# Optimization experiments

Hardware: AMD Instinct MI355X
Metric: run time of the kernel (lower is better)

## Reference

```python
import jax, jax.numpy as jnp
import numpy as np

H = 32  # hidden_size

def _lstm_layer(x, Wih, Whh, bih, bhh):
    """Single LSTM layer, batch_first x: [B,T,I] -> hs [B,T,H].
    PyTorch gate order: i, f, g, o."""
    B = x.shape[0]
    # Precompute all input projections at once: [B,T,4H] -> time-major [T,B,4H]
    xp = (jnp.einsum('bti,gi->btg', x, Wih) + bih + bhh).transpose(1, 0, 2)
    h0 = jnp.zeros((B, H), dtype=x.dtype)
    c0 = jnp.zeros((B, H), dtype=x.dtype)

    def step(carry, xt):
        h, c = carry
        gates = xt + h @ Whh.T                      # [B,4H]
        i, f, g, o = jnp.split(gates, 4, axis=-1)
        i = jax.nn.sigmoid(i)
        f = jax.nn.sigmoid(f)
        g = jnp.tanh(g)
        o = jax.nn.sigmoid(o)
        c = f * c + i * g
        h = o * jnp.tanh(c)
        return (h, c), h

    _, hs = jax.lax.scan(step, (h0, c0), xp)        # hs: [T,B,H]
    return hs.transpose(1, 0, 2)                    # [B,T,H]


def setup_inputs() -> dict:
    key = jax.random.key(0)
    ks = jax.random.split(key, 12)
    B, T, I = 4096, 512, 1
    s = 1.0 / np.sqrt(H)  # PyTorch uniform(-1/sqrt(H), 1/sqrt(H)) init scale
    u = lambda k, shape: jax.random.uniform(k, shape, jnp.float32, -s, s)
    return {
        'x': jax.random.normal(ks[0], (B, T, I), jnp.float32),
        'W_ih_l0': u(ks[1], (4 * H, I)),
        'W_hh_l0': u(ks[2], (4 * H, H)),
        'b_ih_l0': u(ks[3], (4 * H,)),
        'b_hh_l0': u(ks[4], (4 * H,)),
        'W_ih_l1': u(ks[5], (4 * H, H)),
        'W_hh_l1': u(ks[6], (4 * H, H)),
        'b_ih_l1': u(ks[7], (4 * H,)),
        'b_hh_l1': u(ks[8], (4 * H,)),
        'W_fc': u(ks[9], (1, H)),
        'b_fc': u(ks[10], (1,)),
    }


def reference(x, W_ih_l0, W_hh_l0, b_ih_l0, b_hh_l0,
              W_ih_l1, W_hh_l1, b_ih_l1, b_hh_l1, W_fc, b_fc):
    h1 = _lstm_layer(x, W_ih_l0, W_hh_l0, b_ih_l0, b_hh_l0)   # [B,T,H]
    h2 = _lstm_layer(h1, W_ih_l1, W_hh_l1, b_ih_l1, b_hh_l1)  # [B,T,H]
    out = h2[:, -1, :] @ W_fc.T + b_fc                        # [B,1]
    return jax.nn.relu(out)
```

## Files before the change

kernel.cpp:

```cpp
#include <hip/hip_runtime.h>
#include <hip/hip_bf16.h>


typedef __attribute__((ext_vector_type(8))) short bf16x8;
typedef __attribute__((ext_vector_type(4))) float f32x4;
typedef __attribute__((ext_vector_type(4))) int   i32x4;

#define HID 32
#define SEQ 512
#define L2E 1.4426950408889634f
#define LSTR 20

static __device__ __forceinline__ float fexp2(float x){ return __builtin_amdgcn_exp2f(x); }
static __device__ __forceinline__ float frcp (float x){ return __builtin_amdgcn_rcpf(x); }
static __device__ __forceinline__ short f2bf(float f){
  unsigned u = __builtin_bit_cast(unsigned, f);
  u = (u + 0x7fffu + ((u >> 16) & 1u)) >> 16;
  return (short)u;
}

#define CELL(gi, gf, gg, go, cvr, hout) do {                         \
  const float I_ = fexp2(gi), G_ = fexp2(gg);                        \
  const float F_ = fexp2(gf), O_ = fexp2(go);                        \
  const float a_ = 1.f + I_, b_ = 1.f + G_, c_ = 1.f + F_;           \
  const float P1_ = a_ * b_;                                         \
  const float R_  = frcp(c_ * P1_);                                  \
  const float fv_ = P1_ * R_;                                        \
  const float ig_ = (G_ - 1.f) * (c_ * R_);                          \
  (cvr) = fmaf(fv_, (cvr), ig_);                                     \
  const float C2_ = fexp2((cvr) * (2.f * L2E));                      \
  (hout) = (C2_ - 1.f) * frcp((1.f + O_) * (1.f + C2_));             \
} while (0)

__global__ __launch_bounds__(512, 2) void lstm2_zs3_kernel(
    const float* __restrict__ x,
    const float* __restrict__ Wih0, const float* __restrict__ Whh0,
    const float* __restrict__ bih0, const float* __restrict__ bhh0,
    const float* __restrict__ Wih1, const float* __restrict__ Whh1,
    const float* __restrict__ bih1, const float* __restrict__ bhh1,
    const float* __restrict__ Wfc, const float* __restrict__ bfc,
    float* __restrict__ out)
{
  const int tid = threadIdx.x;
  const int w   = tid >> 6;
  const int l   = tid & 63;
  const int m   = l >> 4;
  const int col = l & 15;
  const int V   = w & 3;
  const bool isL1 = (w >= 4);

  __shared__ int   bufH0[4][16 * LSTR];
  __shared__ int   bufH1[2][16 * LSTR];
  __shared__ float bufFC[4][16];

  for (int i = tid; i < 4 * 16 * LSTR; i += 512) ((int*)bufH0)[i] = 0;
  for (int i = tid; i < 2 * 16 * LSTR; i += 512) ((int*)bufH1)[i] = 0;
  __syncthreads();

  const float* Wrec = isL1 ? Whh1 : Whh0;
  const float* Bi   = isL1 ? bih1 : bih0;
  const float* Bh   = isL1 ? bhh1 : bhh0;
  const int   gcol  = col & 3;
  const float scA   = (gcol == 2) ? (2.0f * L2E) : (-L2E);
  bf16x8 wfR[2], wfI[2];
  f32x4  cb[2];
  float  w0x[2][4];
  #pragma unroll
  for (int t = 0; t < 2; ++t) {
    const int ga = gcol * 32 + 8 * V + 2 * (col >> 2) + t;
    #pragma unroll
    for (int j = 0; j < 8; ++j) {
      wfR[t][j] = f2bf(scA * Wrec[ga * HID + (8 * m + j)]);
      wfI[t][j] = isL1 ? f2bf(scA * Wih1[ga * HID + (8 * m + j)]) : (short)0;
    }
    const int uc = 8 * V + 2 * m + t;
    #pragma unroll
    for (int rr = 0; rr < 4; ++rr) {
      const float sc = (rr == 2) ? (2.0f * L2E) : (-L2E);
      cb[t][rr]  = sc * (Bi[rr * 32 + uc] + Bh[rr * 32 + uc]);
      w0x[t][rr] = isL1 ? 0.f : sc * Wih0[rr * 32 + uc];
    }
  }
  const float wfcA = isL1 ? Wfc[8 * V + 2 * m]     : 0.f;
  const float wfcB = isL1 ? Wfc[8 * V + 2 * m + 1] : 0.f;

  float cvA = 0.f, cvB = 0.f, hA = 0.f, hB = 0.f;
  i32x4 h0pre = {0, 0, 0, 0};
  const float* xb = x + (size_t)(blockIdx.x * 16 + col) * SEQ;
  const int  rd = col * LSTR + 4 * m;
  const int  wb = col * LSTR + 4 * V + m;

  float4 xcur = {0.f, 0.f, 0.f, 0.f};
  if (!isL1) xcur = *reinterpret_cast<const float4*>(xb);

  for (int k = 0; k < SEQ / 4; ++k) {
    float4 xnext = {0.f, 0.f, 0.f, 0.f};
    if (!isL1 && k + 1 < SEQ / 4)
      xnext = *reinterpret_cast<const float4*>(xb + (k + 1) * 4);
    #pragma unroll
    for (int uu = 0; uu < 4; ++uu) {
      if (!isL1) {
        const i32x4 hv = *(const i32x4*)&bufH0[(uu + 3) & 3][rd];
        const bf16x8 hf = __builtin_bit_cast(bf16x8, hv);
        const float xt = (uu == 0) ? xcur.x : (uu == 1) ? xcur.y
                       : (uu == 2) ? xcur.z : xcur.w;
        f32x4 cbx0, cbx1;
        #pragma unroll
        for (int rr = 0; rr < 4; ++rr) {
          cbx0[rr] = fmaf(w0x[0][rr], xt, cb[0][rr]);
          cbx1[rr] = fmaf(w0x[1][rr], xt, cb[1][rr]);
        }
        f32x4 A0, A1;
        A0 = __builtin_amdgcn_mfma_f32_16x16x32_bf16(wfR[0], hf, cbx0, 0, 0, 0);
        A1 = __builtin_amdgcn_mfma_f32_16x16x32_bf16(wfR[1], hf, cbx1, 0, 0, 0);
        CELL(A0[0], A0[1], A0[2], A0[3], cvA, hA);
        CELL(A1[0], A1[1], A1[2], A1[3], cvB, hB);
        int pk;
        asm("v_cvt_pk_bf16_f32 %0, %1, %2" : "=v"(pk) : "v"(hA), "v"(hB));
        bufH0[uu][wb] = pk;
      } else {
        const bool doC = (uu >= 2) || (k > 0);
        const bool doP = (uu >= 1) || (k > 0);
        i32x4 h1v = {0, 0, 0, 0};
        if (doC) h1v = *(const i32x4*)&bufH1[(uu + 1) & 1][rd];
        i32x4 h0next = h0pre;
        if (doP) h0next = *(const i32x4*)&bufH0[(uu + 3) & 3][rd];
        if (doC) {
          const bf16x8 h0f = __builtin_bit_cast(bf16x8, h0pre);
          const bf16x8 h1f = __builtin_bit_cast(bf16x8, h1v);
          const f32x4 z4 = {0.f, 0.f, 0.f, 0.f};
          f32x4 P0, P1, Q0, Q1;
          __builtin_amdgcn_s_setprio(1);
          P0 = __builtin_amdgcn_mfma_f32_16x16x32_bf16(wfI[0], h0f, cb[0], 0, 0, 0);
          P1 = __builtin_amdgcn_mfma_f32_16x16x32_bf16(wfI[1], h0f, cb[1], 0, 0, 0);
          Q0 = __builtin_amdgcn_mfma_f32_16x16x32_bf16(wfR[0], h1f, z4, 0, 0, 0);
          Q1 = __builtin_amdgcn_mfma_f32_16x16x32_bf16(wfR[1], h1f, z4, 0, 0, 0);
          __builtin_amdgcn_s_setprio(0);
          const f32x4 A0 = P0 + Q0;
          const f32x4 A1 = P1 + Q1;
          CELL(A0[0], A0[1], A0[2], A0[3], cvA, hA);
          CELL(A1[0], A1[1], A1[2], A1[3], cvB, hB);
          int pk;
          asm("v_cvt_pk_bf16_f32 %0, %1, %2" : "=v"(pk) : "v"(hA), "v"(hB));
          bufH1[uu & 1][wb] = pk;
        }
        h0pre = h0next;
      }
      __syncthreads();
    }
    xcur = xnext;
  }

  if (isL1) {
    const i32x4 h1v = *(const i32x4*)&bufH1[1][rd];
    const bf16x8 h0f = __builtin_bit_cast(bf16x8, h0pre);
    const bf16x8 h1f = __builtin_bit_cast(bf16x8, h1v);
    f32x4 A0, A1;
    A0 = __builtin_amdgcn_mfma_f32_16x16x32_bf16(wfI[0], h0f, cb[0], 0, 0, 0);
    A1 = __builtin_amdgcn_mfma_f32_16x16x32_bf16(wfI[1], h0f, cb[1], 0, 0, 0);
    A0 = __builtin_amdgcn_mfma_f32_16x16x32_bf16(wfR[0], h1f, A0, 0, 0, 0);
    A1 = __builtin_amdgcn_mfma_f32_16x16x32_bf16(wfR[1], h1f, A1, 0, 0, 0);
    CELL(A0[0], A0[1], A0[2], A0[3], cvA, hA);
    CELL(A1[0], A1[1], A1[2], A1[3], cvB, hB);
    int pk;
    asm("v_cvt_pk_bf16_f32 %0, %1, %2" : "=v"(pk) : "v"(hA), "v"(hB));
    bufH1[0][wb] = pk;
  }
  __syncthreads();
  if (isL1) {
    const i32x4 h0v = *(const i32x4*)&bufH0[3][rd];
    const i32x4 h1v = *(const i32x4*)&bufH1[0][rd];
    const bf16x8 h0f = __builtin_bit_cast(bf16x8, h0v);
    const bf16x8 h1f = __builtin_bit_cast(bf16x8, h1v);
    f32x4 A0, A1;
    A0 = __builtin_amdgcn_mfma_f32_16x16x32_bf16(wfI[0], h0f, cb[0], 0, 0, 0);
    A1 = __builtin_amdgcn_mfma_f32_16x16x32_bf16(wfI[1], h0f, cb[1], 0, 0, 0);
    A0 = __builtin_amdgcn_mfma_f32_16x16x32_bf16(wfR[0], h1f, A0, 0, 0, 0);
    A1 = __builtin_amdgcn_mfma_f32_16x16x32_bf16(wfR[1], h1f, A1, 0, 0, 0);
    CELL(A0[0], A0[1], A0[2], A0[3], cvA, hA);
    CELL(A1[0], A1[1], A1[2], A1[3], cvB, hB);
    float part = hA * wfcA + hB * wfcB;
    part += __shfl_xor(part, 16);
    part += __shfl_xor(part, 32);
    if (l < 16) bufFC[V][l] = part;
  }
  __syncthreads();
  if (w == 4 && l < 16) {
    const float o = bufFC[0][l] + bufFC[1][l] + bufFC[2][l] + bufFC[3][l] + bfc[0];
    out[blockIdx.x * 16 + l] = o > 0.f ? o : 0.f;
  }
}

extern "C" void kernel_launch(void* const* d_in, const int* in_sizes, int n_in,
                              void* d_out, int out_size, void* d_ws, size_t ws_size,
                              hipStream_t stream) {
  const float* x    = (const float*)d_in[0];
  const float* Wih0 = (const float*)d_in[1];
  const float* Whh0 = (const float*)d_in[2];
  const float* bih0 = (const float*)d_in[3];
  const float* bhh0 = (const float*)d_in[4];
  const float* Wih1 = (const float*)d_in[5];
  const float* Whh1 = (const float*)d_in[6];
  const float* bih1 = (const float*)d_in[7];
  const float* bhh1 = (const float*)d_in[8];
  const float* Wfc  = (const float*)d_in[9];
  const float* bfc  = (const float*)d_in[10];

  const int B = 4096;
  const int grid = B / 16;
  lstm2_zs3_kernel<<<grid, 512, 0, stream>>>(
      x, Wih0, Whh0, bih0, bhh0, Wih1, Whh1, bih1, bhh1, Wfc, bfc,
      (float*)d_out);
}
```

Measured before the change: 176.5 us.

## Halve batch per block and split cell work across MFMA column halves

Each block now handles 8 sequences instead of 16. The two halves of the MFMA N-columns (q=0/1) duplicate the same sequences, and each lane evaluates one LSTM cell instead of two. A ds_swizzle pairs the hidden values for bf16 packing. The grid doubles and launch bounds raise occupancy to 4 blocks per CU, aiming to shorten the per-step serial cell latency and to hide the per-timestep barriers with more resident blocks. The cost is twice as many MFMA issues overall, since half of each MFMA output is redundant, plus extra register pressure from the occupancy target.

```diff
diff --git a/kernel.cpp b/kernel.cpp
--- a/kernel.cpp
+++ b/kernel.cpp
@@ -32,7 +32,13 @@
   (hout) = (C2_ - 1.f) * frcp((1.f + O_) * (1.f + C2_));             \
 } while (0)
 
-__global__ __launch_bounds__(512, 2) void lstm2_zs3_kernel(
+#define HPACK(hv, pk) do {                                                    \
+  const int pa_ = __builtin_amdgcn_ds_swizzle(__builtin_bit_cast(int, (hv)), 0x201F); \
+  asm("v_cvt_pk_bf16_f32 %0, %1, %2" : "=v"(pk)                               \
+      : "v"(hv), "v"(__builtin_bit_cast(float, pa_)));                        \
+} while (0)
+
+__global__ __launch_bounds__(512, 4) void lstm2_db2_kernel(
     const float* __restrict__ x,
     const float* __restrict__ Wih0, const float* __restrict__ Whh0,
     const float* __restrict__ bih0, const float* __restrict__ bhh0,
@@ -46,15 +52,18 @@
   const int l   = tid & 63;
   const int m   = l >> 4;
   const int col = l & 15;
+  const int q   = col >> 3;
+  const int s   = col & 7;
   const int V   = w & 3;
   const bool isL1 = (w >= 4);
-
-  __shared__ int   bufH0[4][16 * LSTR];
-  __shared__ int   bufH1[2][16 * LSTR];
-  __shared__ float bufFC[4][16];
-
-  for (int i = tid; i < 4 * 16 * LSTR; i += 512) ((int*)bufH0)[i] = 0;
-  for (int i = tid; i < 2 * 16 * LSTR; i += 512) ((int*)bufH1)[i] = 0;
+  const bool qb = (q != 0);
+
+  __shared__ int   bufH0[4][8 * LSTR];
+  __shared__ int   bufH1[2][8 * LSTR];
+  __shared__ float bufFC[4][8];
+
+  for (int i = tid; i < 4 * 8 * LSTR; i += 512) ((int*)bufH0)[i] = 0;
+  for (int i = tid; i < 2 * 8 * LSTR; i += 512) ((int*)bufH1)[i] = 0;
   __syncthreads();
 
   const float* Wrec = isL1 ? Whh1 : Whh0;
@@ -81,14 +90,14 @@
       w0x[t][rr] = isL1 ? 0.f : sc * Wih0[rr * 32 + uc];
     }
   }
-  const float wfcA = isL1 ? Wfc[8 * V + 2 * m]     : 0.f;
-  const float wfcB = isL1 ? Wfc[8 * V + 2 * m + 1] : 0.f;
-
-  float cvA = 0.f, cvB = 0.f, hA = 0.f, hB = 0.f;
+  const float wfc = isL1 ? Wfc[8 * V + 2 * m + q] : 0.f;
+
+  float cv = 0.f, hn = 0.f;
   i32x4 h0pre = {0, 0, 0, 0};
-  const float* xb = x + (size_t)(blockIdx.x * 16 + col) * SEQ;
-  const int  rd = col * LSTR + 4 * m;
-  const int  wb = col * LSTR + 4 * V + m;
+  const float* xb = x + (size_t)(blockIdx.x * 8 + s) * SEQ;
+  const int  rd = s * LSTR + 4 * m;
+  const int  wb = s * LSTR + 4 * V + m;
+  const bool wr = (q == 0);
 
   float4 xcur = {0.f, 0.f, 0.f, 0.f};
   if (!isL1) xcur = *reinterpret_cast<const float4*>(xb);
@@ -113,11 +122,11 @@
         f32x4 A0, A1;
         A0 = __builtin_amdgcn_mfma_f32_16x16x32_bf16(wfR[0], hf, cbx0, 0, 0, 0);
         A1 = __builtin_amdgcn_mfma_f32_16x16x32_bf16(wfR[1], hf, cbx1, 0, 0, 0);
-        CELL(A0[0], A0[1], A0[2], A0[3], cvA, hA);
-        CELL(A1[0], A1[1], A1[2], A1[3], cvB, hB);
+        const f32x4 A = qb ? A1 : A0;
+        CELL(A[0], A[1], A[2], A[3], cv, hn);
         int pk;
-        asm("v_cvt_pk_bf16_f32 %0, %1, %2" : "=v"(pk) : "v"(hA), "v"(hB));
-        bufH0[uu][wb] = pk;
+        HPACK(hn, pk);
+        if (wr) bufH0[uu][wb] = pk;
       } else {
         const bool doC = (uu >= 2) || (k > 0);
         const bool doP = (uu >= 1) || (k > 0);
@@ -138,11 +147,11 @@
           __builtin_amdgcn_s_setprio(0);
           const f32x4 A0 = P0 + Q0;
           const f32x4 A1 = P1 + Q1;
-          CELL(A0[0], A0[1], A0[2], A0[3], cvA, hA);
-          CELL(A1[0], A1[1], A1[2], A1[3], cvB, hB);
+          const f32x4 A = qb ? A1 : A0;
+          CELL(A[0], A[1], A[2], A[3], cv, hn);
           int pk;
-          asm("v_cvt_pk_bf16_f32 %0, %1, %2" : "=v"(pk) : "v"(hA), "v"(hB));
-          bufH1[uu & 1][wb] = pk;
+          HPACK(hn, pk);
+          if (wr) bufH1[uu & 1][wb] = pk;
         }
         h0pre = h0next;
       }
@@ -160,11 +169,11 @@
     A1 = __builtin_amdgcn_mfma_f32_16x16x32_bf16(wfI[1], h0f, cb[1], 0, 0, 0);
     A0 = __builtin_amdgcn_mfma_f32_16x16x32_bf16(wfR[0], h1f, A0, 0, 0, 0);
     A1 = __builtin_amdgcn_mfma_f32_16x16x32_bf16(wfR[1], h1f, A1, 0, 0, 0);
-    CELL(A0[0], A0[1], A0[2], A0[3], cvA, hA);
-    CELL(A1[0], A1[1], A1[2], A1[3], cvB, hB);
+    const f32x4 A = qb ? A1 : A0;
+    CELL(A[0], A[1], A[2], A[3], cv, hn);
     int pk;
-    asm("v_cvt_pk_bf16_f32 %0, %1, %2" : "=v"(pk) : "v"(hA), "v"(hB));
-    bufH1[0][wb] = pk;
+    HPACK(hn, pk);
+    if (wr) bufH1[0][wb] = pk;
   }
   __syncthreads();
   if (isL1) {
@@ -177,17 +186,18 @@
     A1 = __builtin_amdgcn_mfma_f32_16x16x32_bf16(wfI[1], h0f, cb[1], 0, 0, 0);
     A0 = __builtin_amdgcn_mfma_f32_16x16x32_bf16(wfR[0], h1f, A0, 0, 0, 0);
     A1 = __builtin_amdgcn_mfma_f32_16x16x32_bf16(wfR[1], h1f, A1, 0, 0, 0);
-    CELL(A0[0], A0[1], A0[2], A0[3], cvA, hA);
-    CELL(A1[0], A1[1], A1[2], A1[3], cvB, hB);
-    float part = hA * wfcA + hB * wfcB;
+    const f32x4 A = qb ? A1 : A0;
+    CELL(A[0], A[1], A[2], A[3], cv, hn);
+    float part = hn * wfc;
+    part += __shfl_xor(part, 8);
     part += __shfl_xor(part, 16);
     part += __shfl_xor(part, 32);
-    if (l < 16) bufFC[V][l] = part;
+    if (l < 8) bufFC[V][l] = part;
   }
   __syncthreads();
-  if (w == 4 && l < 16) {
+  if (w == 4 && l < 8) {
     const float o = bufFC[0][l] + bufFC[1][l] + bufFC[2][l] + bufFC[3][l] + bfc[0];
-    out[blockIdx.x * 16 + l] = o > 0.f ? o : 0.f;
+    out[blockIdx.x * 8 + l] = o > 0.f ? o : 0.f;
   }
 }
 
@@ -207,8 +217,8 @@
   const float* bfc  = (const float*)d_in[10];
 
   const int B = 4096;
-  const int grid = B / 16;
-  lstm2_zs3_kernel<<<grid, 512, 0, stream>>>(
+  const int grid = B / 8;
+  lstm2_db2_kernel<<<grid, 512, 0, stream>>>(
       x, Wih0, Whh0, bih0, bhh0, Wih1, Whh1, bih1, bhh1, Wfc, bfc,
       (float*)d_out);
 }
```

After: 239.2 us. +35.6%, slower.
